# Kernel tuning notes

Hardware: AMD Instinct MI355X
Metric: run time of the kernel (lower is better)

Reference implementation:

```python
import jax, jax.numpy as jnp
import numpy as np

B, S, D, H = 4, 1024, 1024, 16
HD = D // H


def setup_inputs() -> dict:
    key = jax.random.key(0)
    ks = jax.random.split(key, 12)
    s = 1.0 / np.sqrt(D)
    inp = {
        'q': jax.random.normal(ks[0], (B, S, D), jnp.float32),
        'k': jax.random.normal(ks[1], (B, S, D), jnp.float32),
        'v': jax.random.normal(ks[2], (B, S, D), jnp.float32),
        'mask': jnp.broadcast_to(jnp.tril(jnp.ones((S, S), jnp.int32)), (B, S, S)),
        'Wq': jax.random.uniform(ks[3], (D, D), jnp.float32, -s, s),
        'bq': jax.random.uniform(ks[4], (D,), jnp.float32, -s, s),
        'Wk': jax.random.uniform(ks[5], (D, D), jnp.float32, -s, s),
        'bk': jax.random.uniform(ks[6], (D,), jnp.float32, -s, s),
        'Wv': jax.random.uniform(ks[7], (D, D), jnp.float32, -s, s),
        'bv': jax.random.uniform(ks[8], (D,), jnp.float32, -s, s),
        'Wo': jax.random.uniform(ks[9], (D, D), jnp.float32, -s, s),
        'bo': jax.random.uniform(ks[10], (D,), jnp.float32, -s, s),
    }
    return inp


def _split_heads(x):
    # [B,S,D] -> [B,H,S,HD]
    b, s, d = x.shape
    return x.reshape(b, s, H, HD).transpose(0, 2, 1, 3)


def reference(q, k, v, mask, Wq, bq, Wk, bk, Wv, bv, Wo, bo):
    # Linear projections (torch Linear: x @ W.T + b) followed by relu
    qh = jax.nn.relu(q @ Wq.T + bq)
    kh = jax.nn.relu(k @ Wk.T + bk)
    vh = jax.nn.relu(v @ Wv.T + bv)
    qh, kh, vh = _split_heads(qh), _split_heads(kh), _split_heads(vh)
    scores = jnp.einsum('bhqd,bhkd->bhqk', qh, kh) / jnp.sqrt(jnp.float32(HD))
    scores = jnp.where(mask[:, None, :, :] == 0, jnp.float32(-1e9), scores)
    attn = jax.nn.softmax(scores, axis=-1)
    y = jnp.einsum('bhqk,bhkd->bhqd', attn, vh)
    y = y.transpose(0, 2, 1, 3).reshape(B, S, D)  # merge heads
    return jax.nn.relu(y @ Wo.T + bo)
```

## Files before the change

kernel.cpp:

```cpp
#include <hip/hip_runtime.h>


using f16    = _Float16;
using f16x4  = __attribute__((ext_vector_type(4))) _Float16;
using f16x8  = __attribute__((ext_vector_type(8))) _Float16;
using f32x4  = __attribute__((ext_vector_type(4))) float;
using f32x16 = __attribute__((ext_vector_type(16))) float;

static constexpr int S = 1024, Dm = 1024, NH = 16, HD = 64;

#if __has_builtin(__builtin_amdgcn_mfma_f32_32x32x16_f16)
#define USE_G32 1
#define MFMA32(ACC, A_, B_) \
    (ACC) = __builtin_amdgcn_mfma_f32_32x32x16_f16((A_), (B_), (ACC), 0, 0, 0)
#else
#define USE_G32 0
#endif

#if __has_builtin(__builtin_amdgcn_mfma_f32_16x16x32_f16) && \
    __has_builtin(__builtin_amdgcn_mfma_f32_16x16x16f16)
#define USE_A16 1
#define MFMA16K32(ACC, A_, B_) \
    (ACC) = __builtin_amdgcn_mfma_f32_16x16x32_f16((A_), (B_), (ACC), 0, 0, 0)
#define MFMA16(ACC, A_, B_) \
    (ACC) = __builtin_amdgcn_mfma_f32_16x16x16f16((A_), (B_), (ACC), 0, 0, 0)
#else
#define USE_A16 0
#endif

#define LO4(v) __builtin_shufflevector((v), (v), 0, 1, 2, 3)
#define HI4(v) __builtin_shufflevector((v), (v), 4, 5, 6, 7)

__device__ __forceinline__ f16x4 cvt4(float4 a) {
    f16x4 r; r[0] = (f16)a.x; r[1] = (f16)a.y; r[2] = (f16)a.z; r[3] = (f16)a.w;
    return r;
}

__device__ __forceinline__ int pcol64(int k) {
#if USE_A16
    return ((k >> 3) & 3) * 16 + ((k >> 5) << 3) + (k & 7);
#else
    return ((k >> 2) & 3) * 16 + ((k >> 4) << 2) + (k & 3);
#endif
}

__device__ __forceinline__ int swz(int row, int col) {
    return (col & ~31) | ((((col >> 3) ^ (row >> 1)) & 3) << 3) | (col & 7);
}

__device__ __forceinline__ void store_out(void* out, int mode, int m, int n, float v) {
    if (mode == 2) {
        ((float*)out)[(size_t)m * Dm + n] = v;
    } else {
        const int b_ = m >> 10, s_ = m & 1023, h_ = n >> 6, hd_ = n & 63;
        const size_t idx = (mode == 0)
            ? (((size_t)(b_ * NH + h_) * S + s_) * HD + pcol64(hd_))
            : (((size_t)(b_ * NH + h_) * HD + hd_) * S + s_);
        ((f16*)out)[idx] = (f16)v;
    }
}

#if __has_builtin(__builtin_amdgcn_global_load_lds)
#define HAS_GLL 1
#else
#define HAS_GLL 0
#endif

__device__ __forceinline__ void gll16(const f16* g, f16* l) {
#if HAS_GLL
    __builtin_amdgcn_global_load_lds(
        (const __attribute__((address_space(1))) void*)g,
        (__attribute__((address_space(3))) void*)l, 16, 0, 0);
#else
    *(uint4*)l = *(const uint4*)g;
#endif
}

__global__ __launch_bounds__(256)
void cvt_w(const float* __restrict__ s0, const float* __restrict__ s1,
           const float* __restrict__ s2, f16* __restrict__ dst)
{
    const int z = blockIdx.y;
    const float* src = (z == 0) ? s0 : (z == 1) ? s1 : s2;
    const int e = blockIdx.x * 256 + threadIdx.x;
    const int n = e >> 8;
    const int k = (e & 255) * 4;
    const float4 v = *(const float4*)(src + (size_t)n * Dm + k);
    *(f16x4*)(dst + (size_t)z * Dm * Dm + (size_t)n * Dm + swz(n, k)) = cvt4(v);
}

template <int ADMA>
__device__ __forceinline__ void gemm_core(const void* __restrict__ A,
                                          const f16* __restrict__ Wf,
                                          const float* __restrict__ bias,
                                          void* __restrict__ out, int mode)
{
    const int tid = threadIdx.x;
    const int bm = blockIdx.x, bn = blockIdx.y;
#if USE_G32
    __shared__ alignas(16) f16 As[3][128][32];
    __shared__ alignas(16) f16 Ws[3][128][32];

    const int lane = tid & 63, wave = tid >> 6;
    const int l31 = lane & 31, kh = lane >> 5;
    const int wm = wave & 3, wn = wave >> 2;

    const int drow = tid >> 2;
    const int dcol = (tid & 3) * 8;
    const f16* Wsrc = Wf + (size_t)(bn * 128 + drow) * Dm + dcol;
    const f16* Asrc = (const f16*)A + (size_t)(bm * 128 + drow) * Dm + dcol;

    auto dma = [&](int k0, int buf) {
        gll16(Wsrc + k0, &Ws[buf][drow][dcol]);
        if (ADMA) gll16(Asrc + k0, &As[buf][drow][dcol]);
    };

    const int ar = tid >> 2, aslot = tid & 3;
    const float* Af = (const float*)A + (size_t)(bm * 128 + ar) * Dm + aslot * 8;

    auto prefA = [&](int k0, float4 (&pa)[2]) {
        pa[0] = *(const float4*)(Af + k0);
        pa[1] = *(const float4*)(Af + k0 + 4);
    };
    auto stageA = [&](int buf, const float4 (&pa)[2]) {
        f16x8 v;
        v[0] = (f16)pa[0].x; v[1] = (f16)pa[0].y; v[2] = (f16)pa[0].z; v[3] = (f16)pa[0].w;
        v[4] = (f16)pa[1].x; v[5] = (f16)pa[1].y; v[6] = (f16)pa[1].z; v[7] = (f16)pa[1].w;
        const int phys = (aslot ^ ((ar >> 1) & 3)) & 3;
        *(f16x8*)&As[buf][ar][phys * 8] = v;
    };

    f32x16 acc[2] = {};

    auto kslice = [&](int buf, int s) {
        const int sl = s * 2 + kh;
        const int rA = wm * 32 + l31;
        const int rB0 = wn * 64 + l31, rB1 = wn * 64 + 32 + l31;
        const f16x8 af  = *(const f16x8*)&As[buf][rA][((sl ^ ((rA >> 1) & 3)) & 3) * 8];
        const f16x8 bf0 = *(const f16x8*)&Ws[buf][rB0][((sl ^ ((rB0 >> 1) & 3)) & 3) * 8];
        const f16x8 bf1 = *(const f16x8*)&Ws[buf][rB1][((sl ^ ((rB1 >> 1) & 3)) & 3) * 8];
        MFMA32(acc[0], af, bf0);
        MFMA32(acc[1], af, bf1);
    };

    constexpr int NIT = Dm / 32;
    float4 paA[2], paB[2];

    if (!ADMA) prefA(0, paA);
    dma(0, 0);
    if (!ADMA) prefA(32, paB);
    dma(32, 1);
    if (!ADMA) stageA(0, paA);

    auto iter = [&](int t, float4 (&pnew)[2], const float4 (&pold)[2]) {
        if (t < NIT - 1) {
            if (ADMA) asm volatile("s_waitcnt vmcnt(2)" ::: "memory");
            else      asm volatile("s_waitcnt vmcnt(3)" ::: "memory");
        } else {
            asm volatile("s_waitcnt vmcnt(0)" ::: "memory");
        }
        asm volatile("s_waitcnt lgkmcnt(0)" ::: "memory");
        __builtin_amdgcn_s_barrier();
        __builtin_amdgcn_sched_barrier(0);
        const int cb = t % 3;
        if (t + 2 < NIT) {
            if (!ADMA) prefA((t + 2) * 32, pnew);
            dma((t + 2) * 32, (t + 2) % 3);
        }
        kslice(cb, 0);
        if (!ADMA && t + 1 < NIT) stageA((t + 1) % 3, pold);
        kslice(cb, 1);
    };

    for (int t = 0; t < NIT; t += 2) {
        iter(t, paA, paB);
        iter(t + 1, paB, paA);
    }

#pragma unroll
    for (int j = 0; j < 2; ++j) {
        const int col = bn * 128 + wn * 64 + j * 32 + l31;
        const float bb = bias[col];
#pragma unroll
        for (int blk = 0; blk < 4; ++blk) {
            const int row0 = bm * 128 + wm * 32 + 8 * blk + 4 * kh;
            if (mode == 1) {
                const int b_ = row0 >> 10, s_ = row0 & 1023;
                const int h_ = col >> 6, hd_ = col & 63;
                f16x4 vv;
#pragma unroll
                for (int r = 0; r < 4; ++r)
                    vv[r] = (f16)fmaxf(acc[j][blk * 4 + r] + bb, 0.0f);
                *(f16x4*)&((f16*)out)[((size_t)(b_ * NH + h_) * HD + hd_) * S + s_] = vv;
            } else {
#pragma unroll
                for (int r = 0; r < 4; ++r)
                    store_out(out, mode, row0 + r, col,
                              fmaxf(acc[j][blk * 4 + r] + bb, 0.0f));
            }
        }
    }
#else
    for (int i = tid; i < 128 * 128; i += 512) {
        const int m = bm * 128 + (i >> 7);
        const int n = bn * 128 + (i & 127);
        float acc = 0.0f;
        for (int k2 = 0; k2 < Dm; ++k2) {
            const float a = ADMA ? (float)((const f16*)A)[(size_t)m * Dm + swz(m, k2)]
                                 : ((const float*)A)[(size_t)m * Dm + k2];
            acc = fmaf(a, (float)Wf[(size_t)n * Dm + swz(n, k2)], acc);
        }
        store_out(out, mode, m, n, fmaxf(acc + bias[n], 0.0f));
    }
#endif
}

__global__ __launch_bounds__(512, 6)
void gemm_qkv(const float* __restrict__ q, const float* __restrict__ k,
              const float* __restrict__ v, const f16* __restrict__ wqkv,
              const float* __restrict__ bq, const float* __restrict__ bk,
              const float* __restrict__ bv,
              f16* __restrict__ qh, f16* __restrict__ kh, f16* __restrict__ vt)
{
    const int z = blockIdx.z;
    const float* A = (z == 0) ? q : (z == 1) ? k : v;
    const float* B = (z == 0) ? bq : (z == 1) ? bk : bv;
    f16* O = (z == 0) ? qh : (z == 1) ? kh : vt;
    gemm_core<0>(A, wqkv + (size_t)z * Dm * Dm, B, O, (z == 2) ? 1 : 0);
}

__global__ __launch_bounds__(512, 2)
void gemm_out(const f16* __restrict__ y, const f16* __restrict__ wo,
              const float* __restrict__ bo, float* __restrict__ out)
{
    gemm_core<1>(y, wo, bo, out, 2);
}

__global__ __launch_bounds__(256)
void attn_fwd(const f16* __restrict__ qh, const f16* __restrict__ kh,
              const f16* __restrict__ vt, f16* __restrict__ y)
{
    const int bz = blockIdx.x;
    const int qt = bz & 15;
    const int h  = (bz >> 4) & 15;
    const int b  = bz >> 8;
    const size_t head = (size_t)(b * NH + h) * S * HD;

#if USE_A16
    __shared__ alignas(16) f16 Ks[2][64][72];
    __shared__ alignas(16) f16 Vs[2][64][72];

    const int tid  = threadIdx.x;
    const int wave = tid >> 6;
    const int lane = tid & 63;
    const int l15  = lane & 15;
    const int quad = lane >> 4;
    const int sr   = tid >> 2;
    const int sc   = (tid & 3) * 16;

    const f16* Qrow = qh + head + (size_t)(qt * 64 + wave * 16 + l15) * HD;
    const f16* Kp   = kh + head;
    const f16* Vp   = vt + head;

    f16x8 aq[2];
    {
        const uint4 q0 = *(const uint4*)(Qrow + quad * 16);
        const uint4 q1 = *(const uint4*)(Qrow + quad * 16 + 8);
        aq[0] = *(f16x8*)&q0;
        aq[1] = *(f16x8*)&q1;
    }

    const int qg = qt * 64 + wave * 16 + l15;
    float m_i = -1e30f, l_i = 0.0f;
    f32x4 acc_o[4] = {};

    uint4 pk[2], pv[2];
    auto pref = [&](int kt) {
        const f16* Kr = Kp + (size_t)(kt * 64 + sr) * HD + sc;
        pk[0] = *(const uint4*)Kr;
        pk[1] = *(const uint4*)(Kr + 8);
        const f16* Vr = Vp + (size_t)sr * S + kt * 64 + sc;
        pv[0] = *(const uint4*)Vr;
        pv[1] = *(const uint4*)(Vr + 8);
    };

    pref(0);
    for (int kt = 0; kt <= qt; ++kt) {
        const int cur = kt & 1;
        *(uint4*)&Ks[cur][sr][sc]     = pk[0];
        *(uint4*)&Ks[cur][sr][sc + 8] = pk[1];
        {
            const int sb = (sc >> 4) * 4;
            *(f16x4*)&Vs[cur][sr][0 * 16 + sb] = *(f16x4*)((f16*)&pv[0]);
            *(f16x4*)&Vs[cur][sr][1 * 16 + sb] = *(f16x4*)((f16*)&pv[0] + 4);
            *(f16x4*)&Vs[cur][sr][2 * 16 + sb] = *(f16x4*)((f16*)&pv[1]);
            *(f16x4*)&Vs[cur][sr][3 * 16 + sb] = *(f16x4*)((f16*)&pv[1] + 4);
        }
        __syncthreads();
        if (kt < qt) pref(kt + 1);

        f32x4 accs[4] = {};
#pragma unroll
        for (int t = 0; t < 4; ++t) {
            const f16x8 k8a = *(const f16x8*)&Ks[cur][t * 16 + l15][quad * 16];
            const f16x8 k8b = *(const f16x8*)&Ks[cur][t * 16 + l15][quad * 16 + 8];
            MFMA16K32(accs[t], k8a, aq[0]);
            MFMA16K32(accs[t], k8b, aq[1]);
        }

        const int key0 = kt * 64 + quad * 4;
#pragma unroll
        for (int t = 0; t < 4; ++t)
#pragma unroll
            for (int r = 0; r < 4; ++r) {
                float sv = accs[t][r] * 0.125f;
                if (key0 + t * 16 + r > qg) sv = -1e9f;
                accs[t][r] = sv;
            }

        float mx = accs[0][0];
#pragma unroll
        for (int t = 0; t < 4; ++t)
#pragma unroll
            for (int r = 0; r < 4; ++r) mx = fmaxf(mx, accs[t][r]);
        mx = fmaxf(mx, __shfl_xor(mx, 16, 64));
        mx = fmaxf(mx, __shfl_xor(mx, 32, 64));
        const float mnew = fmaxf(m_i, mx);
        float sm = 0.0f;
#pragma unroll
        for (int t = 0; t < 4; ++t)
#pragma unroll
            for (int r = 0; r < 4; ++r) {
                const float e = __expf(accs[t][r] - mnew);
                accs[t][r] = e;
                sm += e;
            }
        sm += __shfl_xor(sm, 16, 64);
        sm += __shfl_xor(sm, 32, 64);
        const float alpha = __expf(m_i - mnew);
        l_i = l_i * alpha + sm;
        m_i = mnew;

        f16x4 ap[4];
#pragma unroll
        for (int c = 0; c < 4; ++c) {
            f16x4 v;
#pragma unroll
            for (int j = 0; j < 4; ++j) v[j] = (f16)accs[c][j];
            ap[c] = v;
        }

        float ar[4];
#pragma unroll
        for (int r = 0; r < 4; ++r) ar[r] = __shfl(alpha, quad * 4 + r, 64);
#pragma unroll
        for (int t2 = 0; t2 < 4; ++t2)
#pragma unroll
            for (int r = 0; r < 4; ++r) acc_o[t2][r] *= ar[r];
#pragma unroll
        for (int t2 = 0; t2 < 4; ++t2) {
            const f16x8 v8a = *(const f16x8*)&Vs[cur][t2 * 16 + l15][quad * 16];
            const f16x8 v8b = *(const f16x8*)&Vs[cur][t2 * 16 + l15][quad * 16 + 8];
            MFMA16(acc_o[t2], ap[0], LO4(v8a));
            MFMA16(acc_o[t2], ap[1], HI4(v8a));
            MFMA16(acc_o[t2], ap[2], LO4(v8b));
            MFMA16(acc_o[t2], ap[3], HI4(v8b));
        }
    }

    float lr[4];
#pragma unroll
    for (int r = 0; r < 4; ++r) lr[r] = __shfl(l_i, quad * 4 + r, 64);
#pragma unroll
    for (int t2 = 0; t2 < 4; ++t2)
#pragma unroll
        for (int r = 0; r < 4; ++r) {
            const int srow = qt * 64 + wave * 16 + quad * 4 + r;
            const int dcol = h * 64 + t2 * 16 + l15;
            y[((size_t)b * S + srow) * Dm + swz(srow, dcol)] =
                (f16)(acc_o[t2][r] / lr[r]);
        }
#else
    const int tid = threadIdx.x;
    if (tid < 64) {
        const int q = qt * 64 + tid;
        const f16* Qr = qh + head + (size_t)q * HD;
        float qv[64];
        for (int d = 0; d < 64; ++d) qv[d] = (float)Qr[pcol64(d)];
        float mx = -1e30f;
        for (int key = 0; key <= q; ++key) {
            const f16* Kr = kh + head + (size_t)key * HD;
            float s = 0.0f;
            for (int d = 0; d < 64; ++d) s = fmaf(qv[d], (float)Kr[pcol64(d)], s);
            mx = fmaxf(mx, s * 0.125f);
        }
        float o[64];
        for (int d = 0; d < 64; ++d) o[d] = 0.0f;
        float l = 0.0f;
        for (int key = 0; key <= q; ++key) {
            const f16* Kr = kh + head + (size_t)key * HD;
            float s = 0.0f;
            for (int d = 0; d < 64; ++d) s = fmaf(qv[d], (float)Kr[pcol64(d)], s);
            const float p = __expf(s * 0.125f - mx);
            l += p;
            for (int d = 0; d < 64; ++d)
                o[d] = fmaf(p, (float)vt[head + (size_t)d * S + key], o[d]);
        }
        for (int d = 0; d < 64; ++d)
            y[((size_t)b * S + q) * Dm + swz(q, h * 64 + d)] = (f16)(o[d] / l);
    }
#endif
}

extern "C" void kernel_launch(void* const* d_in, const int* in_sizes, int n_in,
                              void* d_out, int out_size, void* d_ws, size_t ws_size,
                              hipStream_t stream)
{
    f16* ws = (f16*)d_ws;
    const size_t SEG = (size_t)4 * 1024 * 1024;
    f16* qh   = ws;
    f16* kh   = ws + SEG;
    f16* vt   = ws + 2 * SEG;
    f16* wqkv = ws + 3 * SEG;
    f16* y    = ws + 3 * SEG;
    f16* wo   = ws;

    cvt_w<<<dim3(1024, 3), 256, 0, stream>>>(
        (const float*)d_in[4], (const float*)d_in[6], (const float*)d_in[8], wqkv);
    gemm_qkv<<<dim3(32, 8, 3), 512, 0, stream>>>(
        (const float*)d_in[0], (const float*)d_in[1], (const float*)d_in[2],
        wqkv,
        (const float*)d_in[5], (const float*)d_in[7], (const float*)d_in[9],
        qh, kh, vt);
    attn_fwd<<<dim3(4 * NH * (S / 64)), 256, 0, stream>>>(qh, kh, vt, y);
    cvt_w<<<dim3(1024, 1), 256, 0, stream>>>(
        (const float*)d_in[10], nullptr, nullptr, wo);
    gemm_out<<<dim3(32, 8), 512, 0, stream>>>(
        y, wo, (const float*)d_in[11], (float*)d_out);
}
```

Baseline: 252.6 us.

## Store weights and attention output in MFMA fragment layout; load GEMM operands directly to registers

Replaces the swizzled row-major f16 layout with a fragment-packed layout (fidx) that matches the 32x32x16 MFMA operand order, so each lane can fetch its operand fragment with one contiguous 16-byte global load. Both GEMMs drop the shared LDS tile pipeline with barriers. The projection GEMM keeps only a small per-wave LDS buffer for the fp32 activations it converts. The output GEMM reads both operands straight from global memory into registers, with no LDS and no barriers. Tiles shrink to 64-row blocks of 256 threads to raise block count, at the cost of losing cross-wave data sharing through LDS, which means more global and L2 traffic.

```diff
diff --git a/kernel.cpp b/kernel.cpp
--- a/kernel.cpp
+++ b/kernel.cpp
@@ -44,36 +44,17 @@
 #endif
 }
 
-__device__ __forceinline__ int swz(int row, int col) {
-    return (col & ~31) | ((((col >> 3) ^ (row >> 1)) & 3) << 3) | (col & 7);
+__device__ __forceinline__ size_t fidx(int r, int k) {
+    return ((size_t)((r >> 5) * 64 + (k >> 4)) * 64
+            + (r & 31) + ((k >> 3) & 1) * 32) * 8 + (k & 7);
 }
 
 __device__ __forceinline__ void store_out(void* out, int mode, int m, int n, float v) {
-    if (mode == 2) {
-        ((float*)out)[(size_t)m * Dm + n] = v;
-    } else {
-        const int b_ = m >> 10, s_ = m & 1023, h_ = n >> 6, hd_ = n & 63;
-        const size_t idx = (mode == 0)
-            ? (((size_t)(b_ * NH + h_) * S + s_) * HD + pcol64(hd_))
-            : (((size_t)(b_ * NH + h_) * HD + hd_) * S + s_);
-        ((f16*)out)[idx] = (f16)v;
-    }
-}
-
-#if __has_builtin(__builtin_amdgcn_global_load_lds)
-#define HAS_GLL 1
-#else
-#define HAS_GLL 0
-#endif
-
-__device__ __forceinline__ void gll16(const f16* g, f16* l) {
-#if HAS_GLL
-    __builtin_amdgcn_global_load_lds(
-        (const __attribute__((address_space(1))) void*)g,
-        (__attribute__((address_space(3))) void*)l, 16, 0, 0);
-#else
-    *(uint4*)l = *(const uint4*)g;
-#endif
+    const int b_ = m >> 10, s_ = m & 1023, h_ = n >> 6, hd_ = n & 63;
+    const size_t idx = (mode == 0)
+        ? (((size_t)(b_ * NH + h_) * S + s_) * HD + pcol64(hd_))
+        : (((size_t)(b_ * NH + h_) * HD + hd_) * S + s_);
+    ((f16*)out)[idx] = (f16)v;
 }
 
 __global__ __launch_bounds__(256)
@@ -83,139 +64,17 @@
     const int z = blockIdx.y;
     const float* src = (z == 0) ? s0 : (z == 1) ? s1 : s2;
     const int e = blockIdx.x * 256 + threadIdx.x;
-    const int n = e >> 8;
-    const int k = (e & 255) * 4;
-    const float4 v = *(const float4*)(src + (size_t)n * Dm + k);
-    *(f16x4*)(dst + (size_t)z * Dm * Dm + (size_t)n * Dm + swz(n, k)) = cvt4(v);
-}
-
-template <int ADMA>
-__device__ __forceinline__ void gemm_core(const void* __restrict__ A,
-                                          const f16* __restrict__ Wf,
-                                          const float* __restrict__ bias,
-                                          void* __restrict__ out, int mode)
-{
-    const int tid = threadIdx.x;
-    const int bm = blockIdx.x, bn = blockIdx.y;
-#if USE_G32
-    __shared__ alignas(16) f16 As[3][128][32];
-    __shared__ alignas(16) f16 Ws[3][128][32];
-
-    const int lane = tid & 63, wave = tid >> 6;
-    const int l31 = lane & 31, kh = lane >> 5;
-    const int wm = wave & 3, wn = wave >> 2;
-
-    const int drow = tid >> 2;
-    const int dcol = (tid & 3) * 8;
-    const f16* Wsrc = Wf + (size_t)(bn * 128 + drow) * Dm + dcol;
-    const f16* Asrc = (const f16*)A + (size_t)(bm * 128 + drow) * Dm + dcol;
-
-    auto dma = [&](int k0, int buf) {
-        gll16(Wsrc + k0, &Ws[buf][drow][dcol]);
-        if (ADMA) gll16(Asrc + k0, &As[buf][drow][dcol]);
-    };
-
-    const int ar = tid >> 2, aslot = tid & 3;
-    const float* Af = (const float*)A + (size_t)(bm * 128 + ar) * Dm + aslot * 8;
-
-    auto prefA = [&](int k0, float4 (&pa)[2]) {
-        pa[0] = *(const float4*)(Af + k0);
-        pa[1] = *(const float4*)(Af + k0 + 4);
-    };
-    auto stageA = [&](int buf, const float4 (&pa)[2]) {
-        f16x8 v;
-        v[0] = (f16)pa[0].x; v[1] = (f16)pa[0].y; v[2] = (f16)pa[0].z; v[3] = (f16)pa[0].w;
-        v[4] = (f16)pa[1].x; v[5] = (f16)pa[1].y; v[6] = (f16)pa[1].z; v[7] = (f16)pa[1].w;
-        const int phys = (aslot ^ ((ar >> 1) & 3)) & 3;
-        *(f16x8*)&As[buf][ar][phys * 8] = v;
-    };
-
-    f32x16 acc[2] = {};
-
-    auto kslice = [&](int buf, int s) {
-        const int sl = s * 2 + kh;
-        const int rA = wm * 32 + l31;
-        const int rB0 = wn * 64 + l31, rB1 = wn * 64 + 32 + l31;
-        const f16x8 af  = *(const f16x8*)&As[buf][rA][((sl ^ ((rA >> 1) & 3)) & 3) * 8];
-        const f16x8 bf0 = *(const f16x8*)&Ws[buf][rB0][((sl ^ ((rB0 >> 1) & 3)) & 3) * 8];
-        const f16x8 bf1 = *(const f16x8*)&Ws[buf][rB1][((sl ^ ((rB1 >> 1) & 3)) & 3) * 8];
-        MFMA32(acc[0], af, bf0);
-        MFMA32(acc[1], af, bf1);
-    };
-
-    constexpr int NIT = Dm / 32;
-    float4 paA[2], paB[2];
-
-    if (!ADMA) prefA(0, paA);
-    dma(0, 0);
-    if (!ADMA) prefA(32, paB);
-    dma(32, 1);
-    if (!ADMA) stageA(0, paA);
-
-    auto iter = [&](int t, float4 (&pnew)[2], const float4 (&pold)[2]) {
-        if (t < NIT - 1) {
-            if (ADMA) asm volatile("s_waitcnt vmcnt(2)" ::: "memory");
-            else      asm volatile("s_waitcnt vmcnt(3)" ::: "memory");
-        } else {
-            asm volatile("s_waitcnt vmcnt(0)" ::: "memory");
-        }
-        asm volatile("s_waitcnt lgkmcnt(0)" ::: "memory");
-        __builtin_amdgcn_s_barrier();
-        __builtin_amdgcn_sched_barrier(0);
-        const int cb = t % 3;
-        if (t + 2 < NIT) {
-            if (!ADMA) prefA((t + 2) * 32, pnew);
-            dma((t + 2) * 32, (t + 2) % 3);
-        }
-        kslice(cb, 0);
-        if (!ADMA && t + 1 < NIT) stageA((t + 1) % 3, pold);
-        kslice(cb, 1);
-    };
-
-    for (int t = 0; t < NIT; t += 2) {
-        iter(t, paA, paB);
-        iter(t + 1, paB, paA);
-    }
-
-#pragma unroll
-    for (int j = 0; j < 2; ++j) {
-        const int col = bn * 128 + wn * 64 + j * 32 + l31;
-        const float bb = bias[col];
-#pragma unroll
-        for (int blk = 0; blk < 4; ++blk) {
-            const int row0 = bm * 128 + wm * 32 + 8 * blk + 4 * kh;
-            if (mode == 1) {
-                const int b_ = row0 >> 10, s_ = row0 & 1023;
-                const int h_ = col >> 6, hd_ = col & 63;
-                f16x4 vv;
-#pragma unroll
-                for (int r = 0; r < 4; ++r)
-                    vv[r] = (f16)fmaxf(acc[j][blk * 4 + r] + bb, 0.0f);
-                *(f16x4*)&((f16*)out)[((size_t)(b_ * NH + h_) * HD + hd_) * S + s_] = vv;
-            } else {
-#pragma unroll
-                for (int r = 0; r < 4; ++r)
-                    store_out(out, mode, row0 + r, col,
-                              fmaxf(acc[j][blk * 4 + r] + bb, 0.0f));
-            }
-        }
-    }
-#else
-    for (int i = tid; i < 128 * 128; i += 512) {
-        const int m = bm * 128 + (i >> 7);
-        const int n = bn * 128 + (i & 127);
-        float acc = 0.0f;
-        for (int k2 = 0; k2 < Dm; ++k2) {
-            const float a = ADMA ? (float)((const f16*)A)[(size_t)m * Dm + swz(m, k2)]
-                                 : ((const float*)A)[(size_t)m * Dm + k2];
-            acc = fmaf(a, (float)Wf[(size_t)n * Dm + swz(n, k2)], acc);
-        }
-        store_out(out, mode, m, n, fmaxf(acc + bias[n], 0.0f));
-    }
-#endif
-}
-
-__global__ __launch_bounds__(512, 6)
+    const int n = e >> 7;
+    const int k0 = (e & 127) * 8;
+    const float4 v0 = *(const float4*)(src + (size_t)n * Dm + k0);
+    const float4 v1 = *(const float4*)(src + (size_t)n * Dm + k0 + 4);
+    f16x8 w;
+    w[0] = (f16)v0.x; w[1] = (f16)v0.y; w[2] = (f16)v0.z; w[3] = (f16)v0.w;
+    w[4] = (f16)v1.x; w[5] = (f16)v1.y; w[6] = (f16)v1.z; w[7] = (f16)v1.w;
+    *(f16x8*)&dst[(size_t)z * Dm * Dm + fidx(n, k0)] = w;
+}
+
+__global__ __launch_bounds__(256, 4)
 void gemm_qkv(const float* __restrict__ q, const float* __restrict__ k,
               const float* __restrict__ v, const f16* __restrict__ wqkv,
               const float* __restrict__ bq, const float* __restrict__ bk,
@@ -224,16 +83,172 @@
 {
     const int z = blockIdx.z;
     const float* A = (z == 0) ? q : (z == 1) ? k : v;
-    const float* B = (z == 0) ? bq : (z == 1) ? bk : bv;
-    f16* O = (z == 0) ? qh : (z == 1) ? kh : vt;
-    gemm_core<0>(A, wqkv + (size_t)z * Dm * Dm, B, O, (z == 2) ? 1 : 0);
-}
-
-__global__ __launch_bounds__(512, 2)
+    const float* bias = (z == 0) ? bq : (z == 1) ? bk : bv;
+    f16* out = (z == 0) ? qh : (z == 1) ? kh : vt;
+    const int mode = (z == 2) ? 1 : 0;
+    const f16* Wf = wqkv + (size_t)z * Dm * Dm;
+
+    const int tid = threadIdx.x;
+    const int bm = blockIdx.x, bn = blockIdx.y;
+#if USE_G32
+    __shared__ alignas(16) f16 Apriv[4][2][2][64][8];
+
+    const int lane = tid & 63, wave = tid >> 6;
+    const int l31 = lane & 31, khh = lane >> 5;
+    const int wm = wave & 1, wn = wave >> 1;
+
+    const float* Af = A + (size_t)(bm * 64 + wm * 32 + (lane >> 1)) * Dm
+                        + (lane & 1) * 16;
+    const f16* Wq0 = Wf + (size_t)(bn * 4 + wn * 2) * 32768 + lane * 8;
+    const f16* Wq1 = Wq0 + 32768;
+
+    auto loadA = [&](int t, float4 (&pa)[4]) {
+#pragma unroll
+        for (int j = 0; j < 4; ++j) pa[j] = *(const float4*)(Af + t * 32 + j * 4);
+    };
+    auto stage = [&](int buf, const float4 (&pa)[4]) {
+        f16x8 lo, hi;
+        lo[0] = (f16)pa[0].x; lo[1] = (f16)pa[0].y; lo[2] = (f16)pa[0].z; lo[3] = (f16)pa[0].w;
+        lo[4] = (f16)pa[1].x; lo[5] = (f16)pa[1].y; lo[6] = (f16)pa[1].z; lo[7] = (f16)pa[1].w;
+        hi[0] = (f16)pa[2].x; hi[1] = (f16)pa[2].y; hi[2] = (f16)pa[2].z; hi[3] = (f16)pa[2].w;
+        hi[4] = (f16)pa[3].x; hi[5] = (f16)pa[3].y; hi[6] = (f16)pa[3].z; hi[7] = (f16)pa[3].w;
+        const int pos = (lane >> 1) + (lane & 1) * 32;
+        *(f16x8*)&Apriv[wave][buf][0][pos][0] = lo;
+        *(f16x8*)&Apriv[wave][buf][1][pos][0] = hi;
+    };
+    auto frag = [&](int buf, int s) -> f16x8 {
+        return *(const f16x8*)&Apriv[wave][buf][khh][l31 + s * 32][0];
+    };
+    auto loadW = [&](int t, f16x8 (&w)[4]) {
+        const f16* p0 = Wq0 + (size_t)t * 1024;
+        const f16* p1 = Wq1 + (size_t)t * 1024;
+        w[0] = *(const f16x8*)p0;
+        w[1] = *(const f16x8*)(p0 + 512);
+        w[2] = *(const f16x8*)p1;
+        w[3] = *(const f16x8*)(p1 + 512);
+    };
+
+    f32x16 acc0 = {}, acc1 = {};
+    constexpr int NIT = Dm / 32;
+
+    float4 a0[4], a1[4];
+    f16x8  w0[4], w1[4];
+    loadA(0, a0); loadW(0, w0);
+    loadA(1, a1); loadW(1, w1);
+    stage(0, a0);
+
+    auto body = [&](int t, float4 (&aD)[4], float4 (&aS)[4], f16x8 (&wU)[4]) {
+        const int rb = t & 1;
+        const f16x8 f0 = frag(rb, 0);
+        const f16x8 f1 = frag(rb, 1);
+        if (t + 2 < NIT) loadA(t + 2, aD);
+        MFMA32(acc0, f0, wU[0]);
+        MFMA32(acc1, f0, wU[2]);
+        MFMA32(acc0, f1, wU[1]);
+        MFMA32(acc1, f1, wU[3]);
+        if (t + 1 < NIT) stage((t + 1) & 1, aS);
+        if (t + 2 < NIT) loadW(t + 2, wU);
+    };
+
+    for (int t = 0; t < NIT; t += 2) {
+        body(t,     a0, a1, w0);
+        body(t + 1, a1, a0, w1);
+    }
+
+#pragma unroll
+    for (int j = 0; j < 2; ++j) {
+        const int col = bn * 128 + wn * 64 + j * 32 + l31;
+        const float bb = bias[col];
+        const f32x16& ac = j ? acc1 : acc0;
+#pragma unroll
+        for (int blk = 0; blk < 4; ++blk) {
+            const int row0 = bm * 64 + wm * 32 + 8 * blk + 4 * khh;
+            if (mode == 1) {
+                const int b_ = row0 >> 10, s_ = row0 & 1023;
+                const int h_ = col >> 6, hd_ = col & 63;
+                f16x4 vv;
+#pragma unroll
+                for (int r = 0; r < 4; ++r)
+                    vv[r] = (f16)fmaxf(ac[blk * 4 + r] + bb, 0.0f);
+                *(f16x4*)&out[((size_t)(b_ * NH + h_) * HD + hd_) * S + s_] = vv;
+            } else {
+#pragma unroll
+                for (int r = 0; r < 4; ++r)
+                    store_out(out, mode, row0 + r, col,
+                              fmaxf(ac[blk * 4 + r] + bb, 0.0f));
+            }
+        }
+    }
+#else
+    for (int i = tid; i < 64 * 128; i += 256) {
+        const int m = bm * 64 + (i >> 7);
+        const int n = bn * 128 + (i & 127);
+        float acc = 0.0f;
+        for (int k2 = 0; k2 < Dm; ++k2)
+            acc = fmaf(A[(size_t)m * Dm + k2], (float)Wf[fidx(n, k2)], acc);
+        store_out(out, mode, m, n, fmaxf(acc + bias[n], 0.0f));
+    }
+#endif
+}
+
+__global__ __launch_bounds__(256, 4)
 void gemm_out(const f16* __restrict__ y, const f16* __restrict__ wo,
               const float* __restrict__ bo, float* __restrict__ out)
 {
-    gemm_core<1>(y, wo, bo, out, 2);
+    const int tid = threadIdx.x;
+    const int bm = blockIdx.x, bn = blockIdx.y;
+#if USE_G32
+    const int lane = tid & 63, wave = tid >> 6;
+    const int l31 = lane & 31, khh = lane >> 5;
+    const int wm = wave & 1, wn = wave >> 1;
+
+    const f16* Ab = y  + (size_t)(bm * 2 + wm) * 32768 + lane * 8;
+    const f16* Wb = wo + (size_t)(bn * 2 + wn) * 32768 + lane * 8;
+
+    auto la = [&](int t, f16x8 (&a)[2]) {
+        a[0] = *(const f16x8*)(Ab + (size_t)t * 1024);
+        a[1] = *(const f16x8*)(Ab + (size_t)t * 1024 + 512);
+    };
+    auto lw = [&](int t, f16x8 (&w)[2]) {
+        w[0] = *(const f16x8*)(Wb + (size_t)t * 1024);
+        w[1] = *(const f16x8*)(Wb + (size_t)t * 1024 + 512);
+    };
+
+    f32x16 acc = {};
+    constexpr int NIT = Dm / 32;
+    f16x8 a0[2], a1[2], w0[2], w1[2];
+    la(0, a0); lw(0, w0);
+    la(1, a1); lw(1, w1);
+
+    auto body = [&](int t, f16x8 (&aU)[2], f16x8 (&wU)[2]) {
+        MFMA32(acc, aU[0], wU[0]);
+        MFMA32(acc, aU[1], wU[1]);
+        if (t + 2 < NIT) { la(t + 2, aU); lw(t + 2, wU); }
+    };
+    for (int t = 0; t < NIT; t += 2) {
+        body(t, a0, w0);
+        body(t + 1, a1, w1);
+    }
+
+    const int col = bn * 64 + wn * 32 + l31;
+    const float bb = bo[col];
+#pragma unroll
+    for (int blk = 0; blk < 4; ++blk) {
+        const int row0 = bm * 64 + wm * 32 + 8 * blk + 4 * khh;
+#pragma unroll
+        for (int r = 0; r < 4; ++r)
+            out[(size_t)(row0 + r) * Dm + col] = fmaxf(acc[blk * 4 + r] + bb, 0.0f);
+    }
+#else
+    for (int i = tid; i < 64 * 64; i += 256) {
+        const int m = bm * 64 + (i >> 6);
+        const int n = bn * 64 + (i & 63);
+        float acc = 0.0f;
+        for (int k2 = 0; k2 < Dm; ++k2)
+            acc = fmaf((float)y[fidx(m, k2)], (float)wo[fidx(n, k2)], acc);
+        out[(size_t)m * Dm + n] = fmaxf(acc + bo[n], 0.0f);
+    }
+#endif
 }
 
 __global__ __launch_bounds__(256)
@@ -377,8 +392,7 @@
         for (int r = 0; r < 4; ++r) {
             const int srow = qt * 64 + wave * 16 + quad * 4 + r;
             const int dcol = h * 64 + t2 * 16 + l15;
-            y[((size_t)b * S + srow) * Dm + swz(srow, dcol)] =
-                (f16)(acc_o[t2][r] / lr[r]);
+            y[fidx(b * S + srow, dcol)] = (f16)(acc_o[t2][r] / lr[r]);
         }
 #else
     const int tid = threadIdx.x;
@@ -407,7 +421,7 @@
                 o[d] = fmaf(p, (float)vt[head + (size_t)d * S + key], o[d]);
         }
         for (int d = 0; d < 64; ++d)
-            y[((size_t)b * S + q) * Dm + swz(q, h * 64 + d)] = (f16)(o[d] / l);
+            y[fidx(b * S + q, h * 64 + d)] = (f16)(o[d] / l);
     }
 #endif
 }
@@ -425,16 +439,16 @@
     f16* y    = ws + 3 * SEG;
     f16* wo   = ws;
 
-    cvt_w<<<dim3(1024, 3), 256, 0, stream>>>(
+    cvt_w<<<dim3(512, 3), 256, 0, stream>>>(
         (const float*)d_in[4], (const float*)d_in[6], (const float*)d_in[8], wqkv);
-    gemm_qkv<<<dim3(32, 8, 3), 512, 0, stream>>>(
+    gemm_qkv<<<dim3(64, 8, 3), 256, 0, stream>>>(
         (const float*)d_in[0], (const float*)d_in[1], (const float*)d_in[2],
         wqkv,
         (const float*)d_in[5], (const float*)d_in[7], (const float*)d_in[9],
         qh, kh, vt);
     attn_fwd<<<dim3(4 * NH * (S / 64)), 256, 0, stream>>>(qh, kh, vt, y);
-    cvt_w<<<dim3(1024, 1), 256, 0, stream>>>(
+    cvt_w<<<dim3(512, 1), 256, 0, stream>>>(
         (const float*)d_in[10], nullptr, nullptr, wo);
-    gemm_out<<<dim3(32, 8), 512, 0, stream>>>(
+    gemm_out<<<dim3(64, 16), 256, 0, stream>>>(
         y, wo, (const float*)d_in[11], (float*)d_out);
 }
```

Measured after the change: 282.2 us. 1.12x slower.
